# Kernel optimization log

Hardware: AMD Instinct MI355X
Metric: run time of the kernel (lower is better)

The kernel has to match this reference:

```python
import jax, jax.numpy as jnp
import numpy as np

B, S, HID = 1, 2048, 7168
NH = 32
Q_LORA, KV_LORA = 1536, 512
ROPE_D, NOPE_D, V_D = 64, 128, 128
SOFTMAX_SCALE = 1.0 / np.sqrt(NOPE_D + ROPE_D)
MIN_MASKED = -10000.0
EPS = 1e-6


def rmsnorm(x, w):
    var = jnp.mean(jnp.square(x), axis=-1, keepdims=True)
    return x * jax.lax.rsqrt(var + EPS) * w


def deinterleave(x):
    # x.view(..., d//2, 2).transpose(-1,-2).reshape(..., d) == concat(even, odd)
    return jnp.concatenate([x[..., 0::2], x[..., 1::2]], axis=-1)


def rotate_half(x):
    d = x.shape[-1] // 2
    return jnp.concatenate([-x[..., d:], x[..., :d]], axis=-1)


def rope_cos_sin(position_ids):
    # standard RoPE table for qk_rope_head_dim, base 10000
    inv_freq = 1.0 / (10000.0 ** (jnp.arange(0, ROPE_D, 2, dtype=jnp.float32) / ROPE_D))
    freqs = position_ids.astype(jnp.float32)[..., None] * inv_freq  # [B,S,ROPE_D/2]
    emb = jnp.concatenate([freqs, freqs], axis=-1)                  # [B,S,ROPE_D]
    return jnp.cos(emb)[:, None], jnp.sin(emb)[:, None]             # [B,1,S,ROPE_D]


def setup_inputs() -> dict:
    key = jax.random.key(0)
    ks = jax.random.split(key, 10)
    w = 0.02
    hidden_states = jax.random.normal(ks[0], (B, S, HID), dtype=jnp.float32)
    # causal mask: True = masked (future positions)
    attention_mask = jnp.triu(jnp.ones((S, S), dtype=bool), k=1)[None, None]
    position_ids = jnp.arange(S, dtype=jnp.int64 if jax.config.x64_enabled else jnp.int32)[None].astype(jnp.int32)
    return {
        "hidden_states": hidden_states,
        "attention_mask": attention_mask,
        "position_ids": position_ids,
        "W_kv_a": jax.random.normal(ks[1], (HID, KV_LORA + ROPE_D), dtype=jnp.float32) * w,
        "W_q_a": jax.random.normal(ks[2], (HID, Q_LORA), dtype=jnp.float32) * w,
        "q_a_ln_w": jnp.ones((Q_LORA,), dtype=jnp.float32),
        "kv_a_ln_w": jnp.ones((KV_LORA,), dtype=jnp.float32),
        "q_rope_w": jax.random.normal(ks[3], (Q_LORA, NH * ROPE_D), dtype=jnp.float32) * w,
        "fusedqk": jax.random.normal(ks[4], (NH, Q_LORA, KV_LORA), dtype=jnp.float32) * w,
        "v_up": jax.random.normal(ks[5], (NH, KV_LORA, V_D), dtype=jnp.float32) * w,
        "W_o": jax.random.normal(ks[6], (NH * V_D, HID), dtype=jnp.float32) * w,
    }


def reference(hidden_states, attention_mask, position_ids, W_kv_a, W_q_a,
              q_a_ln_w, kv_a_ln_w, q_rope_w, fusedqk, v_up, W_o):
    b, s, _ = hidden_states.shape
    # latent projections
    compressed = hidden_states @ W_kv_a                      # [B,S,KV_LORA+ROPE_D]
    kva = rmsnorm(compressed[..., :KV_LORA], kv_a_ln_w)      # [B,S,KV_LORA]
    k_pe = compressed[..., KV_LORA:][:, None]                # [B,1,S,ROPE_D]
    q_a = rmsnorm(hidden_states @ W_q_a, q_a_ln_w)           # [B,S,Q_LORA]
    # rope part of q
    q_pe = (q_a @ q_rope_w).reshape(b, s, NH, ROPE_D).transpose(0, 2, 1, 3)  # [B,H,S,ROPE_D]
    # interleaved RoPE (deinterleave then standard rotate-half)
    cos, sin = rope_cos_sin(position_ids)
    q_pe = deinterleave(q_pe)
    k_pe = deinterleave(k_pe)
    q_pe = q_pe * cos + rotate_half(q_pe) * sin
    k_pe = k_pe * cos + rotate_half(k_pe) * sin
    # weight-absorbed nope query: q_a @ (q_up @ k_up^T) lands in latent space
    dq = jnp.einsum('bsr,hrc->bhsc', q_a, fusedqk)           # [B,H,S,KV_LORA]
    q_full = jnp.concatenate([dq, q_pe], axis=-1)            # [B,H,S,KV_LORA+ROPE_D]
    k_full = jnp.concatenate([kva, k_pe[:, 0]], axis=-1)     # [B,S,KV_LORA+ROPE_D]
    logits = jnp.einsum('bhsc,btc->bhst', q_full, k_full) * SOFTMAX_SCALE
    logits = jnp.where(attention_mask, jnp.float32(MIN_MASKED), logits)
    probs = jax.nn.softmax(logits.astype(jnp.float32), axis=-1).astype(q_full.dtype)
    ctx = jnp.einsum('bhst,btc->bhsc', probs, kva)           # [B,H,S,KV_LORA]
    out = jnp.einsum('bhsc,hcd->bhsd', ctx, v_up)            # [B,H,S,V_D]
    out = out.transpose(0, 2, 1, 3).reshape(b, s, NH * V_D)
    return out @ W_o                                          # [B,S,HID]
```

## Files before the change

### kernel.cpp

```cpp
#include <hip/hip_runtime.h>

typedef unsigned short bf16_t;
typedef __attribute__((ext_vector_type(8))) short short8;
typedef __attribute__((ext_vector_type(4))) float f32x4;

#define S_LEN 2048
#define HID 7168
#define NHEAD 32
#define QLORA 1536
#define KVLORA 512
#define ROPE_DIM 64
#define KFULL 576
#define KFULLP 640
#define V_DIM 128
#define OUTW 4096
#define SM_SCALE 0.07216878364870323f
#define LN10000 9.210340371976184f

__device__ __forceinline__ bf16_t f2bf(float x) {
  unsigned int u = __float_as_uint(x);
  u += 0x7fffu + ((u >> 16) & 1u);
  return (bf16_t)(u >> 16);
}

__device__ __forceinline__ void store_out(float* p, float v) { *p = v; }
__device__ __forceinline__ void store_out(bf16_t* p, float v) { *p = f2bf(v); }

__device__ __forceinline__ void gl_lds16(const bf16_t* g, bf16_t* l) {
  __builtin_amdgcn_global_load_lds(
      (const __attribute__((address_space(1))) void*)g,
      (__attribute__((address_space(3))) void*)l, 16, 0, 0);
}

template<typename CT>
__global__ __launch_bounds__(256) void gemm_bt(
    const bf16_t* __restrict__ A, int lda, long sA,
    const bf16_t* __restrict__ BT, int ldb, long sB,
    CT* __restrict__ C, int ldc, long sC,
    int K, int flags)
{
  __shared__ bf16_t As[128 * 32];
  __shared__ bf16_t Bs[128 * 32];
  const int tid = threadIdx.x;
  const int wid = tid >> 6;
  const int lane = tid & 63;
  const long m0 = (long)blockIdx.y * 128;
  const long n0 = (long)blockIdx.x * 128;
  if ((flags & 1) && n0 >= m0 + 128) return;
  const int z = blockIdx.z;
  A  += (long)z * sA;
  BT += (long)z * sB;
  C  += (long)z * sC;
  int Ke = K;
  if (flags & 2) { int cap = (int)m0 + 128; Ke = cap < K ? cap : K; }

  const int wr = wid >> 1, wc = wid & 1;
  const int srow = lane >> 2;
  const int scol = (lane & 3) * 8;
  const int frow = lane & 15;
  const int fcol = (lane >> 4) * 8;

  f32x4 acc[4][4];
#pragma unroll
  for (int m = 0; m < 4; ++m)
#pragma unroll
    for (int n = 0; n < 4; ++n) acc[m][n] = (f32x4){0.f, 0.f, 0.f, 0.f};

  const bf16_t* Abase = A + m0 * lda;
  const bf16_t* Bbase = BT + n0 * ldb;

  for (int k0 = 0; k0 < Ke; k0 += 32) {
#pragma unroll
    for (int i = 0; i < 2; ++i) {
      const int r = wid * 32 + i * 16;
      gl_lds16(Abase + (long)(r + srow) * lda + k0 + scol, &As[r * 32]);
      gl_lds16(Bbase + (long)(r + srow) * ldb + k0 + scol, &Bs[r * 32]);
    }
    __syncthreads();
    short8 af[4], bfr[4];
#pragma unroll
    for (int m = 0; m < 4; ++m)
      af[m] = *(const short8*)&As[(wr * 64 + m * 16 + frow) * 32 + fcol];
#pragma unroll
    for (int n = 0; n < 4; ++n)
      bfr[n] = *(const short8*)&Bs[(wc * 64 + n * 16 + frow) * 32 + fcol];
#pragma unroll
    for (int m = 0; m < 4; ++m)
#pragma unroll
      for (int n = 0; n < 4; ++n)
        acc[m][n] = __builtin_amdgcn_mfma_f32_16x16x32_bf16(af[m], bfr[n], acc[m][n], 0, 0, 0);
    __syncthreads();
  }

  const int crow = (lane >> 4) * 4;
  const int ccol = lane & 15;
#pragma unroll
  for (int m = 0; m < 4; ++m)
#pragma unroll
    for (int n = 0; n < 4; ++n) {
      long row = m0 + wr * 64 + m * 16 + crow;
      long col = n0 + wc * 64 + n * 16 + ccol;
#pragma unroll
      for (int r = 0; r < 4; ++r)
        store_out(&C[(row + r) * ldc + col], acc[m][n][r]);
    }
}

__global__ __launch_bounds__(256) void trans_f32_bf16(
    const float* __restrict__ in, bf16_t* __restrict__ out, int R, int C, int Cout)
{
  __shared__ float t[32][33];
  const long z = blockIdx.z;
  in  += z * (long)R * C;
  out += z * (long)Cout * R;
  const int r0 = blockIdx.x * 32, c0 = blockIdx.y * 32;
  const int tx = threadIdx.x & 31, ty = threadIdx.x >> 5;
#pragma unroll
  for (int i = 0; i < 4; ++i) {
    int r = r0 + ty + i * 8, c = c0 + tx;
    float v = 0.f;
    if (r < R && c < C) v = in[(long)r * C + c];
    t[ty + i * 8][tx] = v;
  }
  __syncthreads();
#pragma unroll
  for (int i = 0; i < 4; ++i) {
    int orow = c0 + ty + i * 8, ocol = r0 + tx;
    if (orow < Cout && ocol < R) out[(long)orow * R + ocol] = f2bf(t[tx][ty + i * 8]);
  }
}

__global__ __launch_bounds__(256) void trans_bf16(
    const bf16_t* __restrict__ in, int ldin, bf16_t* __restrict__ out, int ldout, int R, int C)
{
  __shared__ bf16_t t[32][33];
  const int r0 = blockIdx.x * 32, c0 = blockIdx.y * 32;
  const int tx = threadIdx.x & 31, ty = threadIdx.x >> 5;
#pragma unroll
  for (int i = 0; i < 4; ++i) {
    int r = r0 + ty + i * 8, c = c0 + tx;
    t[ty + i * 8][tx] = (r < R && c < C) ? in[(long)r * ldin + c] : (bf16_t)0;
  }
  __syncthreads();
#pragma unroll
  for (int i = 0; i < 4; ++i) {
    int orow = c0 + ty + i * 8, ocol = r0 + tx;
    if (orow < C && ocol < R) out[(long)orow * ldout + ocol] = t[tx][ty + i * 8];
  }
}

__global__ __launch_bounds__(256) void cvt_f32_bf16(
    const float* __restrict__ in, bf16_t* __restrict__ out, long n4)
{
  long i = (long)blockIdx.x * 256 + threadIdx.x;
  if (i >= n4) return;
  const float4 v = ((const float4*)in)[i];
  ushort4 o;
  o.x = f2bf(v.x); o.y = f2bf(v.y); o.z = f2bf(v.z); o.w = f2bf(v.w);
  ((ushort4*)out)[i] = o;
}

__device__ __forceinline__ float block_sum(float v) {
#pragma unroll
  for (int o = 32; o > 0; o >>= 1) v += __shfl_xor(v, o);
  __shared__ float sh[4];
  __syncthreads();
  if ((threadIdx.x & 63) == 0) sh[threadIdx.x >> 6] = v;
  __syncthreads();
  return sh[0] + sh[1] + sh[2] + sh[3];
}
__device__ __forceinline__ float block_max(float v) {
#pragma unroll
  for (int o = 32; o > 0; o >>= 1) v = fmaxf(v, __shfl_xor(v, o));
  __shared__ float sh[4];
  __syncthreads();
  if ((threadIdx.x & 63) == 0) sh[threadIdx.x >> 6] = v;
  __syncthreads();
  return fmaxf(fmaxf(sh[0], sh[1]), fmaxf(sh[2], sh[3]));
}

__global__ __launch_bounds__(256) void rmsnorm_k(
    const float* __restrict__ in, int ldin, const float* __restrict__ w,
    bf16_t* __restrict__ out, int ldout, int len)
{
  const long r = blockIdx.x;
  const float* x = in + r * ldin;
  float ss = 0.f;
  for (int c = threadIdx.x; c < len; c += 256) { float v = x[c]; ss += v * v; }
  ss = block_sum(ss);
  const float sc = rsqrtf(ss / len + 1e-6f);
  for (int c = threadIdx.x; c < len; c += 256)
    out[r * ldout + c] = f2bf(x[c] * sc * w[c]);
}

__global__ __launch_bounds__(256) void softmax_causal(
    const float* __restrict__ logits, bf16_t* __restrict__ probs)
{
  __shared__ float buf[S_LEN];
  const int r = blockIdx.x;
  const long z = blockIdx.y;
  const float* L = logits + (z * S_LEN + r) * (long)S_LEN;
  bf16_t* P = probs + (z * S_LEN + r) * (long)S_LEN;
  const int n = r + 1;
  float mx = -1e30f;
  for (int c = threadIdx.x; c < n; c += 256) {
    float v = L[c] * SM_SCALE;
    buf[c] = v;
    mx = fmaxf(mx, v);
  }
  mx = block_max(mx);
  float sum = 0.f;
  for (int c = threadIdx.x; c < n; c += 256) {
    float e = __expf(buf[c] - mx);
    buf[c] = e;
    sum += e;
  }
  sum = block_sum(sum);
  const float inv = 1.f / sum;
  for (int c = threadIdx.x; c < S_LEN; c += 256)
    P[c] = f2bf(c < n ? buf[c] * inv : 0.f);
}

__global__ __launch_bounds__(256) void rope_q_k(
    const float* __restrict__ qpe, const int* __restrict__ pos_ids, bf16_t* __restrict__ qfull)
{
  const int s = blockIdx.x;
  const float pos = (float)pos_ids[s];
  for (int idx = threadIdx.x; idx < NHEAD * 32; idx += 256) {
    const int h = idx >> 5, i = idx & 31;
    const float* xr = qpe + (long)s * 2048 + h * 64;
    float x0 = xr[2 * i], x1 = xr[2 * i + 1];
    float invf = __expf(-(float)(2 * i) * (LN10000 / 64.f));
    float f = pos * invf;
    float cs = cosf(f), sn = sinf(f);
    bf16_t* o = qfull + (long)h * (S_LEN * KFULL) + (long)s * KFULL + KVLORA;
    o[i]      = f2bf(x0 * cs - x1 * sn);
    o[i + 32] = f2bf(x1 * cs + x0 * sn);
  }
}

__global__ void rope_k_k(
    const float* __restrict__ comp, const int* __restrict__ pos_ids, bf16_t* __restrict__ kfull)
{
  const int s = blockIdx.x;
  const int i = threadIdx.x;
  if (i >= 32) return;
  const float pos = (float)pos_ids[s];
  const float* xr = comp + (long)s * KFULLP + KVLORA;
  float x0 = xr[2 * i], x1 = xr[2 * i + 1];
  float invf = __expf(-(float)(2 * i) * (LN10000 / 64.f));
  float f = pos * invf;
  float cs = cosf(f), sn = sinf(f);
  bf16_t* o = kfull + (long)s * KFULL + KVLORA;
  o[i]      = f2bf(x0 * cs - x1 * sn);
  o[i + 32] = f2bf(x1 * cs + x0 * sn);
}

extern "C" void kernel_launch(void* const* d_in, const int* in_sizes, int n_in,
                              void* d_out, int out_size, void* d_ws, size_t ws_size,
                              hipStream_t stream)
{
  const float* hs    = (const float*)d_in[0];
  const int*   pos   = (const int*)d_in[2];
  const float* Wkva  = (const float*)d_in[3];
  const float* Wqa   = (const float*)d_in[4];
  const float* qlnw  = (const float*)d_in[5];
  const float* kvlnw = (const float*)d_in[6];
  const float* Wqr   = (const float*)d_in[7];
  const float* fqk   = (const float*)d_in[8];
  const float* vupw  = (const float*)d_in[9];
  const float* Wo    = (const float*)d_in[10];
  float* out = (float*)d_out;
  (void)in_sizes; (void)n_in; (void)out_size; (void)ws_size;

  char* cur = (char*)d_ws;
  auto alloc = [&](size_t bytes) -> void* {
    void* p = (void*)cur;
    cur += (bytes + 255) & ~(size_t)255;
    return p;
  };
  bf16_t* hsB    = (bf16_t*)alloc((size_t)S_LEN * HID * 2);
  bf16_t* WkvaT  = (bf16_t*)alloc((size_t)KFULLP * HID * 2);
  bf16_t* WqaT   = (bf16_t*)alloc((size_t)QLORA * HID * 2);
  bf16_t* WqrT   = (bf16_t*)alloc((size_t)2048 * QLORA * 2);
  bf16_t* fqkT   = (bf16_t*)alloc((size_t)NHEAD * KVLORA * QLORA * 2);
  bf16_t* vupT   = (bf16_t*)alloc((size_t)NHEAD * V_DIM * KVLORA * 2);
  bf16_t* WoT    = (bf16_t*)alloc((size_t)HID * OUTW * 2);
  float*  comp   = (float*)alloc((size_t)S_LEN * KFULLP * 4);
  float*  qaraw  = (float*)alloc((size_t)S_LEN * QLORA * 4);
  bf16_t* qaB    = (bf16_t*)alloc((size_t)S_LEN * QLORA * 2);
  bf16_t* kfull  = (bf16_t*)alloc((size_t)S_LEN * KFULL * 2);
  bf16_t* kvaT   = (bf16_t*)alloc((size_t)KVLORA * S_LEN * 2);
  float*  qperaw = (float*)alloc((size_t)S_LEN * 2048 * 4);
  bf16_t* qfull  = (bf16_t*)alloc((size_t)NHEAD * S_LEN * KFULL * 2);
  float*  logits = (float*)alloc((size_t)4 * S_LEN * S_LEN * 4);
  bf16_t* probs  = (bf16_t*)alloc((size_t)4 * S_LEN * S_LEN * 2);
  bf16_t* attno  = (bf16_t*)alloc((size_t)S_LEN * OUTW * 2);

  cvt_f32_bf16<<<(int)(((long)S_LEN * HID / 4 + 255) / 256), 256, 0, stream>>>(hs, hsB, (long)S_LEN * HID / 4);
  trans_f32_bf16<<<dim3(HID / 32, KFULLP / 32, 1), 256, 0, stream>>>(Wkva, WkvaT, HID, KFULL, KFULLP);
  trans_f32_bf16<<<dim3(HID / 32, QLORA / 32, 1), 256, 0, stream>>>(Wqa, WqaT, HID, QLORA, QLORA);
  trans_f32_bf16<<<dim3(QLORA / 32, 2048 / 32, 1), 256, 0, stream>>>(Wqr, WqrT, QLORA, 2048, 2048);
  trans_f32_bf16<<<dim3(QLORA / 32, KVLORA / 32, NHEAD), 256, 0, stream>>>(fqk, fqkT, QLORA, KVLORA, KVLORA);
  trans_f32_bf16<<<dim3(KVLORA / 32, V_DIM / 32, NHEAD), 256, 0, stream>>>(vupw, vupT, KVLORA, V_DIM, V_DIM);
  trans_f32_bf16<<<dim3(OUTW / 32, HID / 32, 1), 256, 0, stream>>>(Wo, WoT, OUTW, HID, HID);

  gemm_bt<float><<<dim3(KFULLP / 128, S_LEN / 128, 1), 256, 0, stream>>>(
      hsB, HID, 0, WkvaT, HID, 0, comp, KFULLP, 0, HID, 0);
  gemm_bt<float><<<dim3(QLORA / 128, S_LEN / 128, 1), 256, 0, stream>>>(
      hsB, HID, 0, WqaT, HID, 0, qaraw, QLORA, 0, HID, 0);

  rmsnorm_k<<<S_LEN, 256, 0, stream>>>(comp, KFULLP, kvlnw, kfull, KFULL, KVLORA);
  rope_k_k<<<S_LEN, 64, 0, stream>>>(comp, pos, kfull);
  rmsnorm_k<<<S_LEN, 256, 0, stream>>>(qaraw, QLORA, qlnw, qaB, QLORA, QLORA);
  trans_bf16<<<dim3(S_LEN / 32, KVLORA / 32, 1), 256, 0, stream>>>(kfull, KFULL, kvaT, S_LEN, S_LEN, KVLORA);

  gemm_bt<float><<<dim3(2048 / 128, S_LEN / 128, 1), 256, 0, stream>>>(
      qaB, QLORA, 0, WqrT, QLORA, 0, qperaw, 2048, 0, QLORA, 0);
  rope_q_k<<<S_LEN, 256, 0, stream>>>(qperaw, pos, qfull);

  gemm_bt<bf16_t><<<dim3(KVLORA / 128, S_LEN / 128, NHEAD), 256, 0, stream>>>(
      qaB, QLORA, 0, fqkT, QLORA, (long)KVLORA * QLORA, qfull, KFULL, (long)S_LEN * KFULL, QLORA, 0);

  for (int ch = 0; ch < 8; ++ch) {
    bf16_t* qh = qfull + (long)ch * 4 * S_LEN * KFULL;
    gemm_bt<float><<<dim3(S_LEN / 128, S_LEN / 128, 4), 256, 0, stream>>>(
        qh, KFULL, (long)S_LEN * KFULL, kfull, KFULL, 0,
        logits, S_LEN, (long)S_LEN * S_LEN, KFULL, 1);
    softmax_causal<<<dim3(S_LEN, 4, 1), 256, 0, stream>>>(logits, probs);
    gemm_bt<bf16_t><<<dim3(KVLORA / 128, S_LEN / 128, 4), 256, 0, stream>>>(
        probs, S_LEN, (long)S_LEN * S_LEN, kvaT, S_LEN, 0,
        qh, KFULL, (long)S_LEN * KFULL, S_LEN, 2);
  }

  gemm_bt<bf16_t><<<dim3(V_DIM / 128, S_LEN / 128, NHEAD), 256, 0, stream>>>(
      qfull, KFULL, (long)S_LEN * KFULL, vupT, KVLORA, (long)V_DIM * KVLORA,
      attno, OUTW, (long)V_DIM, KVLORA, 0);

  gemm_bt<float><<<dim3(HID / 128, S_LEN / 128, 1), 256, 0, stream>>>(
      attno, OUTW, 0, WoT, OUTW, 0, out, HID, 0, OUTW, 0);
}
```

Baseline: 2.126 ms.

## Replace chunked logits/softmax/PV GEMMs with fused causal flash-attention MLA kernel

Replaces the per-4-head loop of full logits GEMM, separate causal softmax and probs·V GEMM with a single flash-attention kernel. It keeps Q fragments in registers, streams 32-row K/V tiles into swizzled LDS and uses online softmax with a lazy rescale threshold. It also skips fully masked KV tiles above the diagonal. This removes the large fp32 logits and bf16 probs round trips through HBM and half of the causal work. The cost is high register pressure (18 Q fragments plus 32 accumulator tiles per lane), small KV tiles and imbalanced causal block work.

```diff
diff --git a/kernel.cpp b/kernel.cpp
--- a/kernel.cpp
+++ b/kernel.cpp
@@ -106,6 +106,136 @@
     }
 }
 
+__global__ __launch_bounds__(256, 2) void flash_mla(
+    const bf16_t* __restrict__ qfull, const bf16_t* __restrict__ kfull,
+    const bf16_t* __restrict__ kvaT, bf16_t* __restrict__ ctx)
+{
+  __shared__ bf16_t Ks[32 * 576];
+  __shared__ bf16_t VTs[512 * 32];
+  const int tid = threadIdx.x;
+  const int wid = tid >> 6, lane = tid & 63;
+  const int l15 = lane & 15, g = lane >> 4;
+  const int qb = 31 - (int)blockIdx.x;
+  const int h = blockIdx.y;
+  const int qg = qb * 64 + wid * 16 + l15;
+
+  short8 Qf[18];
+  {
+    const bf16_t* qrow = qfull + ((long)h * S_LEN + qg) * KFULL + g * 8;
+#pragma unroll
+    for (int ks = 0; ks < 18; ++ks)
+      Qf[ks] = *(const short8*)(qrow + 32 * ks);
+  }
+  f32x4 O[32];
+#pragma unroll
+  for (int j = 0; j < 32; ++j) O[j] = (f32x4){0.f, 0.f, 0.f, 0.f};
+  float m = -3e38f, l = 0.f;
+
+  const int nt = 2 * qb + 2;
+  for (int t = 0; t < nt; ++t) {
+    const int kv0 = 32 * t;
+#pragma unroll
+    for (int i = 0; i < 9; ++i) {
+      const int c = wid * 9 + i;
+      const int u = c * 64 + lane;
+      const int r = u / 72, sl = u % 72;
+      const int gsl = sl ^ (r & 7);
+      gl_lds16(kfull + (long)(kv0 + r) * KFULL + gsl * 8, &Ks[c * 512]);
+    }
+#pragma unroll
+    for (int i = 0; i < 8; ++i) {
+      const int c = wid * 8 + i;
+      const int u = c * 64 + lane;
+      const int r = u >> 2, sl = u & 3;
+      const int gsl = sl ^ ((r >> 1) & 3);
+      gl_lds16(kvaT + (long)r * S_LEN + kv0 + gsl * 8, &VTs[c * 512]);
+    }
+    __syncthreads();
+
+    f32x4 S0 = {0.f, 0.f, 0.f, 0.f}, S1 = {0.f, 0.f, 0.f, 0.f};
+    __builtin_amdgcn_s_setprio(1);
+#pragma unroll
+    for (int ks = 0; ks < 18; ++ks) {
+      {
+        const int r = l15;
+        const short8 af = *(const short8*)&Ks[r * 576 + (((4 * ks + g) ^ (r & 7)) * 8)];
+        S0 = __builtin_amdgcn_mfma_f32_16x16x32_bf16(af, Qf[ks], S0, 0, 0, 0);
+      }
+      {
+        const int r = 16 + l15;
+        const short8 af = *(const short8*)&Ks[r * 576 + (((4 * ks + g) ^ (r & 7)) * 8)];
+        S1 = __builtin_amdgcn_mfma_f32_16x16x32_bf16(af, Qf[ks], S1, 0, 0, 0);
+      }
+    }
+    __builtin_amdgcn_s_setprio(0);
+
+    float s[8];
+    float pm = -3e38f;
+#pragma unroll
+    for (int f = 0; f < 2; ++f)
+#pragma unroll
+      for (int rg = 0; rg < 4; ++rg) {
+        float v = (f ? S1[rg] : S0[rg]) * SM_SCALE;
+        const int kg = kv0 + 16 * f + 4 * g + rg;
+        if (kg > qg) v = -3e38f;
+        s[f * 4 + rg] = v;
+        pm = fmaxf(pm, v);
+      }
+    pm = fmaxf(pm, __shfl_xor(pm, 16));
+    pm = fmaxf(pm, __shfl_xor(pm, 32));
+    if (!__all(pm <= m + 8.f)) {
+      const float mn = fmaxf(m, pm);
+      const float sc = __expf(m - mn);
+      m = mn; l *= sc;
+#pragma unroll
+      for (int j = 0; j < 32; ++j) {
+        O[j][0] *= sc; O[j][1] *= sc; O[j][2] *= sc; O[j][3] *= sc;
+      }
+    }
+    float p[8], psum = 0.f;
+#pragma unroll
+    for (int e = 0; e < 8; ++e) { p[e] = __expf(s[e] - m); psum += p[e]; }
+    psum += __shfl_xor(psum, 16);
+    psum += __shfl_xor(psum, 32);
+    l += psum;
+
+    unsigned int u0f0 = (unsigned)f2bf(p[0]) | ((unsigned)f2bf(p[1]) << 16);
+    unsigned int u1f0 = (unsigned)f2bf(p[2]) | ((unsigned)f2bf(p[3]) << 16);
+    unsigned int u0f1 = (unsigned)f2bf(p[4]) | ((unsigned)f2bf(p[5]) << 16);
+    unsigned int u1f1 = (unsigned)f2bf(p[6]) | ((unsigned)f2bf(p[7]) << 16);
+    const int srcA = l15 + 16 * (2 * (g & 1));
+    const int srcB = srcA + 16;
+    const unsigned int a0 = __shfl(u0f0, srcA), a1 = __shfl(u1f0, srcA);
+    const unsigned int a2 = __shfl(u0f0, srcB), a3 = __shfl(u1f0, srcB);
+    const unsigned int b0 = __shfl(u0f1, srcA), b1 = __shfl(u1f1, srcA);
+    const unsigned int b2 = __shfl(u0f1, srcB), b3 = __shfl(u1f1, srcB);
+    union { unsigned int u[4]; short8 v; } pb;
+    const bool hi = (g >> 1) != 0;
+    pb.u[0] = hi ? b0 : a0; pb.u[1] = hi ? b1 : a1;
+    pb.u[2] = hi ? b2 : a2; pb.u[3] = hi ? b3 : a3;
+
+    const int vsl = (g ^ ((l15 >> 1) & 3)) * 8;
+    __builtin_amdgcn_s_setprio(1);
+#pragma unroll
+    for (int j = 0; j < 32; ++j) {
+      const short8 av = *(const short8*)&VTs[(16 * j + l15) * 32 + vsl];
+      O[j] = __builtin_amdgcn_mfma_f32_16x16x32_bf16(av, pb.v, O[j], 0, 0, 0);
+    }
+    __builtin_amdgcn_s_setprio(0);
+    __syncthreads();
+  }
+
+  const float inv = 1.f / l;
+  bf16_t* orow = ctx + ((long)h * S_LEN + qg) * KVLORA;
+#pragma unroll
+  for (int j = 0; j < 32; ++j) {
+    ushort4 w;
+    w.x = f2bf(O[j][0] * inv); w.y = f2bf(O[j][1] * inv);
+    w.z = f2bf(O[j][2] * inv); w.w = f2bf(O[j][3] * inv);
+    *(ushort4*)(orow + 16 * j + 4 * g) = w;
+  }
+}
+
 __global__ __launch_bounds__(256) void trans_f32_bf16(
     const float* __restrict__ in, bf16_t* __restrict__ out, int R, int C, int Cout)
 {
@@ -168,15 +298,6 @@
   if ((threadIdx.x & 63) == 0) sh[threadIdx.x >> 6] = v;
   __syncthreads();
   return sh[0] + sh[1] + sh[2] + sh[3];
-}
-__device__ __forceinline__ float block_max(float v) {
-#pragma unroll
-  for (int o = 32; o > 0; o >>= 1) v = fmaxf(v, __shfl_xor(v, o));
-  __shared__ float sh[4];
-  __syncthreads();
-  if ((threadIdx.x & 63) == 0) sh[threadIdx.x >> 6] = v;
-  __syncthreads();
-  return fmaxf(fmaxf(sh[0], sh[1]), fmaxf(sh[2], sh[3]));
 }
 
 __global__ __launch_bounds__(256) void rmsnorm_k(
@@ -191,34 +312,6 @@
   const float sc = rsqrtf(ss / len + 1e-6f);
   for (int c = threadIdx.x; c < len; c += 256)
     out[r * ldout + c] = f2bf(x[c] * sc * w[c]);
-}
-
-__global__ __launch_bounds__(256) void softmax_causal(
-    const float* __restrict__ logits, bf16_t* __restrict__ probs)
-{
-  __shared__ float buf[S_LEN];
-  const int r = blockIdx.x;
-  const long z = blockIdx.y;
-  const float* L = logits + (z * S_LEN + r) * (long)S_LEN;
-  bf16_t* P = probs + (z * S_LEN + r) * (long)S_LEN;
-  const int n = r + 1;
-  float mx = -1e30f;
-  for (int c = threadIdx.x; c < n; c += 256) {
-    float v = L[c] * SM_SCALE;
-    buf[c] = v;
-    mx = fmaxf(mx, v);
-  }
-  mx = block_max(mx);
-  float sum = 0.f;
-  for (int c = threadIdx.x; c < n; c += 256) {
-    float e = __expf(buf[c] - mx);
-    buf[c] = e;
-    sum += e;
-  }
-  sum = block_sum(sum);
-  const float inv = 1.f / sum;
-  for (int c = threadIdx.x; c < S_LEN; c += 256)
-    P[c] = f2bf(c < n ? buf[c] * inv : 0.f);
 }
 
 __global__ __launch_bounds__(256) void rope_q_k(
@@ -293,8 +386,7 @@
   bf16_t* kvaT   = (bf16_t*)alloc((size_t)KVLORA * S_LEN * 2);
   float*  qperaw = (float*)alloc((size_t)S_LEN * 2048 * 4);
   bf16_t* qfull  = (bf16_t*)alloc((size_t)NHEAD * S_LEN * KFULL * 2);
-  float*  logits = (float*)alloc((size_t)4 * S_LEN * S_LEN * 4);
-  bf16_t* probs  = (bf16_t*)alloc((size_t)4 * S_LEN * S_LEN * 2);
+  bf16_t* ctxB   = (bf16_t*)alloc((size_t)NHEAD * S_LEN * KVLORA * 2);
   bf16_t* attno  = (bf16_t*)alloc((size_t)S_LEN * OUTW * 2);
 
   cvt_f32_bf16<<<(int)(((long)S_LEN * HID / 4 + 255) / 256), 256, 0, stream>>>(hs, hsB, (long)S_LEN * HID / 4);
@@ -322,19 +414,10 @@
   gemm_bt<bf16_t><<<dim3(KVLORA / 128, S_LEN / 128, NHEAD), 256, 0, stream>>>(
       qaB, QLORA, 0, fqkT, QLORA, (long)KVLORA * QLORA, qfull, KFULL, (long)S_LEN * KFULL, QLORA, 0);
 
-  for (int ch = 0; ch < 8; ++ch) {
-    bf16_t* qh = qfull + (long)ch * 4 * S_LEN * KFULL;
-    gemm_bt<float><<<dim3(S_LEN / 128, S_LEN / 128, 4), 256, 0, stream>>>(
-        qh, KFULL, (long)S_LEN * KFULL, kfull, KFULL, 0,
-        logits, S_LEN, (long)S_LEN * S_LEN, KFULL, 1);
-    softmax_causal<<<dim3(S_LEN, 4, 1), 256, 0, stream>>>(logits, probs);
-    gemm_bt<bf16_t><<<dim3(KVLORA / 128, S_LEN / 128, 4), 256, 0, stream>>>(
-        probs, S_LEN, (long)S_LEN * S_LEN, kvaT, S_LEN, 0,
-        qh, KFULL, (long)S_LEN * KFULL, S_LEN, 2);
-  }
+  flash_mla<<<dim3(32, 32), 256, 0, stream>>>(qfull, kfull, kvaT, ctxB);
 
   gemm_bt<bf16_t><<<dim3(V_DIM / 128, S_LEN / 128, NHEAD), 256, 0, stream>>>(
-      qfull, KFULL, (long)S_LEN * KFULL, vupT, KVLORA, (long)V_DIM * KVLORA,
+      ctxB, KVLORA, (long)S_LEN * KVLORA, vupT, KVLORA, (long)V_DIM * KVLORA,
       attno, OUTW, (long)V_DIM, KVLORA, 0);
 
   gemm_bt<float><<<dim3(HID / 128, S_LEN / 128, 1), 256, 0, stream>>>(
```

Result: slower. 2.371 ms (+11.6%).
